# Performance work log

Measured on AMD Instinct MI355X. Metric: run time of the kernel, lower is better.

## Reference

```python
import jax, jax.numpy as jnp
import numpy as np

HEADS = 16
EPS = 1e-6

def _rmsnorm(x, g):
    # x: (..., d); norm = ||x||_2 * d^-0.5 (matches torch.norm-based RMSNorm)
    d = x.shape[-1]
    nrm = jnp.linalg.norm(x, axis=-1, keepdims=True) * (d ** -0.5)
    return x / (nrm + EPS) * g

def _rope(x, cos, sin):
    # x: (b,n,h,d) -> complex pairs over last dim; cos/sin: (1,n,1,d//2)
    b, n, h, d = x.shape
    xr = x.reshape(b, n, h, d // 2, 2)
    re, im = xr[..., 0], xr[..., 1]
    out_re = re * cos - im * sin
    out_im = re * sin + im * cos
    return jnp.stack([out_re, out_im], axis=-1).reshape(b, n, h, d)

def setup_inputs() -> dict:
    key = jax.random.key(0)
    ks = jax.random.split(key, 8)
    b, n, dim = 4, 4096, 1024
    d = dim // HEADS
    x = jax.random.normal(ks[0], (b, n, dim), dtype=jnp.float32)
    # rope freqs as cos/sin of random angles (broadcast shape 1,n,1,d//2)
    ang = jax.random.uniform(ks[1], (1, n, 1, d // 2), dtype=jnp.float32) * (2 * np.pi)
    freqs_cos = jnp.cos(ang)
    freqs_sin = jnp.sin(ang)
    sc = dim ** -0.5
    w_qkv = jax.random.normal(ks[2], (dim, 3 * dim), dtype=jnp.float32) * sc
    g_q = jnp.ones((d,), dtype=jnp.float32)
    g_k = jnp.ones((d,), dtype=jnp.float32)
    w_proj = jax.random.normal(ks[3], (dim, dim), dtype=jnp.float32) * sc
    b_proj = jnp.zeros((dim,), dtype=jnp.float32)
    return {"x": x, "freqs_cos": freqs_cos, "freqs_sin": freqs_sin,
            "w_qkv": w_qkv, "g_q": g_q, "g_k": g_k,
            "w_proj": w_proj, "b_proj": b_proj}

def reference(x, freqs_cos, freqs_sin, w_qkv, g_q, g_k, w_proj, b_proj):
    b, n, dim = x.shape
    h = HEADS
    d = dim // h
    scale = d ** -0.5
    qkv = x @ w_qkv  # (b,n,3*dim)
    q, k, v = jnp.split(qkv, 3, axis=-1)
    q = q.reshape(b, n, h, d)
    k = k.reshape(b, n, h, d)
    v = v.reshape(b, n, h, d)
    q = _rmsnorm(q, g_q)
    k = _rmsnorm(k, g_k)
    q = _rope(q, freqs_cos, freqs_sin)
    k = _rope(k, freqs_cos, freqs_sin)
    # per-token head-mixing attention: (b,n,h,h)
    attn = jnp.einsum('bnhd,bngd->bnhg', q, k) * scale
    attn = jax.nn.softmax(attn, axis=-1)
    out = jnp.einsum('bnhg,bngd->bnhd', attn, v).reshape(b, n, dim)
    return out @ w_proj + b_proj
```

## Files before the change

kernel.cpp:

```cpp
#include <hip/hip_runtime.h>
#include <hip/hip_bf16.h>
#include <stddef.h>

#define NTOK   16384
#define SEQN   4096
#define DIM    1024
#define K3     3072
#define HEADS  16
#define HD     64

typedef __attribute__((ext_vector_type(8)))  short  short8;
typedef __attribute__((ext_vector_type(4)))  float  float4v;

static __device__ __forceinline__ unsigned short f32_to_bf16_bits(float f) {
    unsigned u = __float_as_uint(f);
    unsigned r = u + 0x7fffu + ((u >> 16) & 1u);
    return (unsigned short)(r >> 16);
}
static __device__ __forceinline__ unsigned pack_bf16x2(float lo, float hi) {
    return (unsigned)f32_to_bf16_bits(lo) | ((unsigned)f32_to_bf16_bits(hi) << 16);
}
static __device__ __forceinline__ void unpack_bf16x8(uint4 u, float* f) {
    f[0] = __uint_as_float(u.x << 16); f[1] = __uint_as_float(u.x & 0xffff0000u);
    f[2] = __uint_as_float(u.y << 16); f[3] = __uint_as_float(u.y & 0xffff0000u);
    f[4] = __uint_as_float(u.z << 16); f[5] = __uint_as_float(u.z & 0xffff0000u);
    f[6] = __uint_as_float(u.w << 16); f[7] = __uint_as_float(u.w & 0xffff0000u);
}

typedef const void __attribute__((address_space(1)))* gas_ptr;
typedef void __attribute__((address_space(3)))* las_ptr;
static __device__ __forceinline__ void gload_lds16(const unsigned short* g,
                                                   unsigned short* l) {
    __builtin_amdgcn_global_load_lds((gas_ptr)g, (las_ptr)l, 16, 0, 0);
}

__global__ void cvt_f32_bf16(const float4* __restrict__ in,
                             ushort4* __restrict__ out, int n4) {
    int i = blockIdx.x * blockDim.x + threadIdx.x;
    if (i < n4) {
        float4 v = in[i];
        ushort4 o;
        o.x = f32_to_bf16_bits(v.x);
        o.y = f32_to_bf16_bits(v.y);
        o.z = f32_to_bf16_bits(v.z);
        o.w = f32_to_bf16_bits(v.w);
        out[i] = o;
    }
}

__global__ void transpose_cvt(const float* __restrict__ in,
                              unsigned short* __restrict__ out,
                              int K, int N) {
    __shared__ float t[32][33];
    int n0 = blockIdx.x * 32, k0 = blockIdx.y * 32;
    int tx = threadIdx.x, ty = threadIdx.y;
    #pragma unroll
    for (int r = ty; r < 32; r += 8)
        t[r][tx] = in[(size_t)(k0 + r) * N + n0 + tx];
    __syncthreads();
    #pragma unroll
    for (int r = ty; r < 32; r += 8)
        out[(size_t)(n0 + r) * K + k0 + tx] = f32_to_bf16_bits(t[tx][r]);
}

template<int WITH_BIAS>
__global__ __launch_bounds__(512, 2) void gemm_bf16_256(
    const unsigned short* __restrict__ A,
    const unsigned short* __restrict__ Bt,
    void* __restrict__ Cout,
    const float* __restrict__ bias,
    int M, int N)
{
    constexpr int K = 1024;
    __shared__ unsigned short As[2][256][64];
    __shared__ unsigned short Bs[2][256][64];

    const int tid  = threadIdx.x;
    const int wave = tid >> 6;
    const int lane = tid & 63;
    const int wm   = wave >> 2;
    const int wn   = wave & 3;
    const int l15  = lane & 15;
    const int l4   = lane >> 4;
    const int l7   = lane & 7;

    const int nwg = (int)gridDim.x;
    const int bid = (int)blockIdx.x;
    const int swz = (bid & 7) * (nwg >> 3) + (bid >> 3);
    const int ntn = N >> 8;
    const int rowBase = (swz / ntn) << 8;
    const int colBase = (swz % ntn) << 8;
    (void)M;

    const int drow = lane >> 3;
    const int lc   = l7 ^ drow;
    const unsigned short* gA = A  + (size_t)(rowBase + drow) * K + lc * 8;
    const unsigned short* gB = Bt + (size_t)(colBase + drow) * K + lc * 8;

    float4v acc[8][4];
    #pragma unroll
    for (int m = 0; m < 8; m++)
        #pragma unroll
        for (int n = 0; n < 4; n++) acc[m][n] = (float4v)0.0f;

    short8 aF[4][2], b0F[2][2], b1F[2][2];

#define STG_A(f, oddH, T) do {                                               \
    const int ra_ = ((wave >> 2) * 128) + (oddH) * 64 + (wave & 3) * 16;     \
    gload_lds16(gA + (size_t)(ra_    ) * K + (size_t)(T) * 64, &As[f][ra_    ][0]); \
    gload_lds16(gA + (size_t)(ra_ + 8) * K + (size_t)(T) * 64, &As[f][ra_ + 8][0]); \
  } while (0)
#define STG_B(f, oddH, T) do {                                               \
    const int rb_ = ((wave >> 1) * 64) + (oddH) * 32 + (wave & 1) * 16;      \
    gload_lds16(gB + (size_t)(rb_    ) * K + (size_t)(T) * 64, &Bs[f][rb_    ][0]); \
    gload_lds16(gB + (size_t)(rb_ + 8) * K + (size_t)(T) * 64, &Bs[f][rb_ + 8][0]); \
  } while (0)

#define RD_A(f, a) do {                                                      \
    _Pragma("unroll")                                                        \
    for (int ra = 0; ra < 4; ra++) {                                         \
      const unsigned short* r_ = &As[f][wm * 128 + (a) * 64 + ra * 16 + l15][0]; \
      aF[ra][0] = *(const short8*)(r_ + (((    l4) ^ l7) * 8));              \
      aF[ra][1] = *(const short8*)(r_ + (((4 + l4) ^ l7) * 8));              \
    } } while (0)
#define RD_B(f, b, dst) do {                                                 \
    _Pragma("unroll")                                                        \
    for (int cb = 0; cb < 2; cb++) {                                         \
      const unsigned short* r_ = &Bs[f][wn * 64 + (b) * 32 + cb * 16 + l15][0]; \
      dst[cb][0] = *(const short8*)(r_ + (((    l4) ^ l7) * 8));             \
      dst[cb][1] = *(const short8*)(r_ + (((4 + l4) ^ l7) * 8));             \
    } } while (0)

#define MM(a, b, bF) do {                                                    \
    _Pragma("unroll")                                                        \
    for (int ra = 0; ra < 4; ra++)                                           \
      _Pragma("unroll")                                                      \
      for (int cb = 0; cb < 2; cb++) {                                       \
        acc[(a)*4+ra][(b)*2+cb] = __builtin_amdgcn_mfma_f32_16x16x32_bf16(   \
            aF[ra][0], bF[cb][0], acc[(a)*4+ra][(b)*2+cb], 0, 0, 0);         \
        acc[(a)*4+ra][(b)*2+cb] = __builtin_amdgcn_mfma_f32_16x16x32_bf16(   \
            aF[ra][1], bF[cb][1], acc[(a)*4+ra][(b)*2+cb], 0, 0, 0);         \
      } } while (0)

#define BAR()   __builtin_amdgcn_s_barrier()
#define VM(n)   asm volatile("s_waitcnt vmcnt(" #n ")" ::: "memory")
#define P1()    __builtin_amdgcn_s_setprio(1)
#define P0()    __builtin_amdgcn_s_setprio(0)

    STG_A(0,0,0); STG_B(0,0,0); STG_B(0,1,0); STG_A(0,1,0);
    STG_A(1,0,1); STG_B(1,0,1); STG_B(1,1,1);
    VM(6);
    BAR();

    #pragma unroll 1
    for (int i = 0; i < 7; i++) {
        const int t1 = 2 * i + 1;
        RD_A(0,0); RD_B(0,0,b0F); STG_A(1,1,t1);
        BAR(); P1(); MM(0,0,b0F); P0(); BAR();
        RD_B(0,1,b1F);            STG_A(0,0,t1+1);
        BAR(); P1(); MM(0,1,b1F); P0(); BAR();
        RD_A(0,1);                STG_B(0,0,t1+1);
        BAR(); P1(); MM(1,1,b1F); P0(); BAR();
                                  STG_B(0,1,t1+1); VM(6);
        BAR(); P1(); MM(1,0,b0F); P0(); BAR();
        RD_A(1,0); RD_B(1,0,b0F); STG_A(0,1,t1+1);
        BAR(); P1(); MM(0,0,b0F); P0(); BAR();
        RD_B(1,1,b1F);            STG_A(1,0,t1+2);
        BAR(); P1(); MM(0,1,b1F); P0(); BAR();
        RD_A(1,1);                STG_B(1,0,t1+2);
        BAR(); P1(); MM(1,1,b1F); P0(); BAR();
                                  STG_B(1,1,t1+2); VM(6);
        BAR(); P1(); MM(1,0,b0F); P0(); BAR();
    }

    {
        RD_A(0,0); RD_B(0,0,b0F); STG_A(1,1,15);
        BAR(); P1(); MM(0,0,b0F); P0(); BAR();
        RD_B(0,1,b1F);
        BAR(); P1(); MM(0,1,b1F); P0(); BAR();
        RD_A(0,1);
        BAR(); P1(); MM(1,1,b1F); P0(); BAR();
        VM(0);
        BAR(); P1(); MM(1,0,b0F); P0(); BAR();
        RD_A(1,0); RD_B(1,0,b0F); P1(); MM(0,0,b0F); P0();
        RD_B(1,1,b1F);            P1(); MM(0,1,b1F); P0();
        RD_A(1,1);                P1(); MM(1,1,b1F); P0();
                                  P1(); MM(1,0,b0F); P0();
    }

    #pragma unroll
    for (int m = 0; m < 8; m++) {
        const int row = rowBase + wm * 128 + m * 16 + l4 * 4;
        #pragma unroll
        for (int n = 0; n < 4; n++) {
            const int col = colBase + wn * 64 + n * 16 + l15;
            if (WITH_BIAS) {
                const float bv = bias[col];
                #pragma unroll
                for (int r = 0; r < 4; r++)
                    ((float*)Cout)[(size_t)(row + r) * N + col] = acc[m][n][r] + bv;
            } else {
                #pragma unroll
                for (int r = 0; r < 4; r++)
                    ((unsigned short*)Cout)[(size_t)(row + r) * N + col] =
                        f32_to_bf16_bits(acc[m][n][r]);
            }
        }
    }
#undef STG_A
#undef STG_B
#undef RD_A
#undef RD_B
#undef MM
#undef BAR
#undef VM
#undef P1
#undef P0
}

__global__ __launch_bounds__(256) void attn_tok(
    const unsigned short* __restrict__ qkv,
    const float* __restrict__ fcos,
    const float* __restrict__ fsin,
    const float* __restrict__ gq,
    const float* __restrict__ gk,
    unsigned short* __restrict__ outb)
{
    __shared__ float kl[4][16][68];
    __shared__ float vl[4][16][68];

    const int tid  = threadIdx.x;
    const int wv   = tid >> 6;
    const int lane = tid & 63;
    const int h    = lane & 15;
    const int p    = lane >> 4;
    const int tok  = blockIdx.x * 4 + wv;
    const int n    = tok & (SEQN - 1);

    const unsigned short* base = qkv + (size_t)tok * K3 + h * 64 + p * 16;
    uint4 qr0 = *(const uint4*)(base);
    uint4 qr1 = *(const uint4*)(base + 8);
    uint4 kr0 = *(const uint4*)(base + DIM);
    uint4 kr1 = *(const uint4*)(base + DIM + 8);
    uint4 vr0 = *(const uint4*)(base + 2 * DIM);
    uint4 vr1 = *(const uint4*)(base + 2 * DIM + 8);

    float q[16], k[16], v[16];
    unpack_bf16x8(qr0, q); unpack_bf16x8(qr1, q + 8);
    unpack_bf16x8(kr0, k); unpack_bf16x8(kr1, k + 8);
    unpack_bf16x8(vr0, v); unpack_bf16x8(vr1, v + 8);

    float ssq = 0.f, ssk = 0.f;
    #pragma unroll
    for (int i = 0; i < 16; i++) { ssq += q[i] * q[i]; ssk += k[i] * k[i]; }
    ssq += __shfl_xor(ssq, 16); ssq += __shfl_xor(ssq, 32);
    ssk += __shfl_xor(ssk, 16); ssk += __shfl_xor(ssk, 32);
    const float sq = 1.0f / (sqrtf(ssq) * 0.125f + 1e-6f);
    const float sk = 1.0f / (sqrtf(ssk) * 0.125f + 1e-6f);

    #pragma unroll
    for (int c = 0; c < 4; c++) {
        float4 gg = *(const float4*)(gq + p * 16 + c * 4);
        float4 gh = *(const float4*)(gk + p * 16 + c * 4);
        q[c*4+0] *= sq * gg.x; q[c*4+1] *= sq * gg.y;
        q[c*4+2] *= sq * gg.z; q[c*4+3] *= sq * gg.w;
        k[c*4+0] *= sk * gh.x; k[c*4+1] *= sk * gh.y;
        k[c*4+2] *= sk * gh.z; k[c*4+3] *= sk * gh.w;
    }

    {
        const float* cb = fcos + n * 32 + p * 8;
        const float* sb = fsin + n * 32 + p * 8;
        float4 c0 = *(const float4*)cb, c1 = *(const float4*)(cb + 4);
        float4 s0 = *(const float4*)sb, s1 = *(const float4*)(sb + 4);
        float cs[8] = {c0.x,c0.y,c0.z,c0.w,c1.x,c1.y,c1.z,c1.w};
        float sn[8] = {s0.x,s0.y,s0.z,s0.w,s1.x,s1.y,s1.z,s1.w};
        #pragma unroll
        for (int j = 0; j < 8; j++) {
            float re = q[2*j], im = q[2*j+1];
            q[2*j]   = re * cs[j] - im * sn[j];
            q[2*j+1] = re * sn[j] + im * cs[j];
            re = k[2*j]; im = k[2*j+1];
            k[2*j]   = re * cs[j] - im * sn[j];
            k[2*j+1] = re * sn[j] + im * cs[j];
        }
    }

    {
        float* krow = &kl[wv][h][p * 16];
        float* vrow = &vl[wv][h][p * 16];
        #pragma unroll
        for (int c = 0; c < 4; c++) {
            *(float4*)(krow + c*4) = make_float4(k[c*4], k[c*4+1], k[c*4+2], k[c*4+3]);
            *(float4*)(vrow + c*4) = make_float4(v[c*4], v[c*4+1], v[c*4+2], v[c*4+3]);
        }
    }

    float s[16];
    #pragma unroll
    for (int g = 0; g < 16; g++) {
        const float* kg = &kl[wv][g][p * 16];
        float4 a0 = *(const float4*)(kg);
        float4 a1 = *(const float4*)(kg + 4);
        float4 a2 = *(const float4*)(kg + 8);
        float4 a3 = *(const float4*)(kg + 12);
        s[g] = q[0]*a0.x + q[1]*a0.y + q[2]*a0.z + q[3]*a0.w
             + q[4]*a1.x + q[5]*a1.y + q[6]*a1.z + q[7]*a1.w
             + q[8]*a2.x + q[9]*a2.y + q[10]*a2.z + q[11]*a2.w
             + q[12]*a3.x + q[13]*a3.y + q[14]*a3.z + q[15]*a3.w;
    }
    #pragma unroll
    for (int g = 0; g < 16; g++) {
        s[g] += __shfl_xor(s[g], 16);
        s[g] += __shfl_xor(s[g], 32);
        s[g] *= 0.125f;
    }

    float m = s[0];
    #pragma unroll
    for (int g = 1; g < 16; g++) m = fmaxf(m, s[g]);
    float sum = 0.f;
    #pragma unroll
    for (int g = 0; g < 16; g++) { s[g] = __expf(s[g] - m); sum += s[g]; }
    const float inv = 1.0f / sum;

    float o[16];
    #pragma unroll
    for (int i = 0; i < 16; i++) o[i] = 0.f;
    #pragma unroll
    for (int g = 0; g < 16; g++) {
        const float pg = s[g] * inv;
        const float* vg = &vl[wv][g][p * 16];
        float4 b0 = *(const float4*)(vg);
        float4 b1 = *(const float4*)(vg + 4);
        float4 b2 = *(const float4*)(vg + 8);
        float4 b3 = *(const float4*)(vg + 12);
        o[0]  += pg * b0.x; o[1]  += pg * b0.y; o[2]  += pg * b0.z; o[3]  += pg * b0.w;
        o[4]  += pg * b1.x; o[5]  += pg * b1.y; o[6]  += pg * b1.z; o[7]  += pg * b1.w;
        o[8]  += pg * b2.x; o[9]  += pg * b2.y; o[10] += pg * b2.z; o[11] += pg * b2.w;
        o[12] += pg * b3.x; o[13] += pg * b3.y; o[14] += pg * b3.z; o[15] += pg * b3.w;
    }

    uint4 r0, r1;
    r0.x = pack_bf16x2(o[0],  o[1]);  r0.y = pack_bf16x2(o[2],  o[3]);
    r0.z = pack_bf16x2(o[4],  o[5]);  r0.w = pack_bf16x2(o[6],  o[7]);
    r1.x = pack_bf16x2(o[8],  o[9]);  r1.y = pack_bf16x2(o[10], o[11]);
    r1.z = pack_bf16x2(o[12], o[13]); r1.w = pack_bf16x2(o[14], o[15]);
    unsigned short* ob = outb + (size_t)tok * DIM + h * 64 + p * 16;
    *(uint4*)(ob)     = r0;
    *(uint4*)(ob + 8) = r1;
}

extern "C" void kernel_launch(void* const* d_in, const int* in_sizes, int n_in,
                              void* d_out, int out_size, void* d_ws, size_t ws_size,
                              hipStream_t stream) {
    const float* x      = (const float*)d_in[0];
    const float* fcos   = (const float*)d_in[1];
    const float* fsin   = (const float*)d_in[2];
    const float* w_qkv  = (const float*)d_in[3];
    const float* g_q    = (const float*)d_in[4];
    const float* g_k    = (const float*)d_in[5];
    const float* w_proj = (const float*)d_in[6];
    const float* b_proj = (const float*)d_in[7];
    float* out = (float*)d_out;

    char* ws = (char*)d_ws;
    unsigned short* xb      = (unsigned short*)(ws);
    unsigned short* wqkvT   = (unsigned short*)(ws + 33554432);
    unsigned short* wprojT  = (unsigned short*)(ws + 39845888);
    unsigned short* qkv     = (unsigned short*)(ws + 41943040);
    unsigned short* attnout = (unsigned short*)(ws + 142606336);
    (void)ws_size; (void)in_sizes; (void)n_in; (void)out_size;

    {
        int n4 = (NTOK * DIM) / 4;
        cvt_f32_bf16<<<(n4 + 255) / 256, 256, 0, stream>>>(
            (const float4*)x, (ushort4*)xb, n4);
        transpose_cvt<<<dim3(K3 / 32, DIM / 32), dim3(32, 8), 0, stream>>>(
            w_qkv, wqkvT, DIM, K3);
        transpose_cvt<<<dim3(DIM / 32, DIM / 32), dim3(32, 8), 0, stream>>>(
            w_proj, wprojT, DIM, DIM);
    }
    gemm_bf16_256<0><<<dim3((NTOK / 256) * (K3 / 256)), 512, 0, stream>>>(
        xb, wqkvT, (void*)qkv, nullptr, NTOK, K3);
    attn_tok<<<NTOK / 4, 256, 0, stream>>>(qkv, fcos, fsin, g_q, g_k, attnout);
    gemm_bf16_256<1><<<dim3((NTOK / 256) * (DIM / 256)), 512, 0, stream>>>(
        attnout, wprojT, (void*)out, b_proj, NTOK, DIM);
}
```

Baseline: 332.8 us.

## Restructure GEMM main loop to overlap LDS reads with MFMA, halve barriers

Reworks the software pipeline of the bf16 MFMA GEMM main loop. Shared-memory fragment reads for the next sub-tile and global-to-LDS staging are now issued right after each MFMA cluster, with one barrier per phase instead of two. The prologue stages one extra tile and preloads the first fragments. Scheduling barriers keep the compiler from reordering across phases. This cuts barrier stalls and hides LDS latency behind MFMA work, but it risks LDS read/write hazards if the buffer-reuse ordering is wrong.

```diff
diff --git a/kernel.cpp b/kernel.cpp
--- a/kernel.cpp
+++ b/kernel.cpp
@@ -143,50 +143,46 @@
       } } while (0)
 
 #define BAR()   __builtin_amdgcn_s_barrier()
+#define SB()    __builtin_amdgcn_sched_barrier(0)
 #define VM(n)   asm volatile("s_waitcnt vmcnt(" #n ")" ::: "memory")
 #define P1()    __builtin_amdgcn_s_setprio(1)
 #define P0()    __builtin_amdgcn_s_setprio(0)
 
     STG_A(0,0,0); STG_B(0,0,0); STG_B(0,1,0); STG_A(0,1,0);
-    STG_A(1,0,1); STG_B(1,0,1); STG_B(1,1,1);
-    VM(6);
+    STG_A(1,0,1); STG_B(1,0,1); STG_B(1,1,1); STG_A(1,1,1);
+    VM(8);
     BAR();
+    RD_A(0,0); RD_B(0,0,b0F);
+    SB(); BAR();
 
     #pragma unroll 1
     for (int i = 0; i < 7; i++) {
-        const int t1 = 2 * i + 1;
-        RD_A(0,0); RD_B(0,0,b0F); STG_A(1,1,t1);
-        BAR(); P1(); MM(0,0,b0F); P0(); BAR();
-        RD_B(0,1,b1F);            STG_A(0,0,t1+1);
-        BAR(); P1(); MM(0,1,b1F); P0(); BAR();
-        RD_A(0,1);                STG_B(0,0,t1+1);
-        BAR(); P1(); MM(1,1,b1F); P0(); BAR();
-                                  STG_B(0,1,t1+1); VM(6);
-        BAR(); P1(); MM(1,0,b0F); P0(); BAR();
-        RD_A(1,0); RD_B(1,0,b0F); STG_A(0,1,t1+1);
-        BAR(); P1(); MM(0,0,b0F); P0(); BAR();
-        RD_B(1,1,b1F);            STG_A(1,0,t1+2);
-        BAR(); P1(); MM(0,1,b1F); P0(); BAR();
-        RD_A(1,1);                STG_B(1,0,t1+2);
-        BAR(); P1(); MM(1,1,b1F); P0(); BAR();
-                                  STG_B(1,1,t1+2); VM(6);
-        BAR(); P1(); MM(1,0,b0F); P0(); BAR();
-    }
-
-    {
-        RD_A(0,0); RD_B(0,0,b0F); STG_A(1,1,15);
-        BAR(); P1(); MM(0,0,b0F); P0(); BAR();
-        RD_B(0,1,b1F);
-        BAR(); P1(); MM(0,1,b1F); P0(); BAR();
-        RD_A(0,1);
-        BAR(); P1(); MM(1,1,b1F); P0(); BAR();
-        VM(0);
-        BAR(); P1(); MM(1,0,b0F); P0(); BAR();
-        RD_A(1,0); RD_B(1,0,b0F); P1(); MM(0,0,b0F); P0();
-        RD_B(1,1,b1F);            P1(); MM(0,1,b1F); P0();
-        RD_A(1,1);                P1(); MM(1,1,b1F); P0();
-                                  P1(); MM(1,0,b0F); P0();
-    }
+        const int T0 = 2 * i + 2, T1 = 2 * i + 3;
+        RD_B(0,1,b1F);                 STG_A(0,0,T0);
+        P1(); MM(0,0,b0F); P0(); SB(); BAR();
+        P1(); MM(0,1,b1F); P0(); RD_A(0,1);  STG_B(0,0,T0); SB(); BAR();
+        P1(); MM(1,1,b1F); P0();             STG_B(0,1,T0); SB(); BAR();
+        P1(); MM(1,0,b0F); P0(); VM(6);
+        RD_A(1,0); RD_B(1,0,b0F);            STG_A(0,1,T0); SB(); BAR();
+        RD_B(1,1,b1F);                 STG_A(1,0,T1);
+        P1(); MM(0,0,b0F); P0(); SB(); BAR();
+        P1(); MM(0,1,b1F); P0(); RD_A(1,1);  STG_B(1,0,T1); SB(); BAR();
+        P1(); MM(1,1,b1F); P0();             STG_B(1,1,T1); SB(); BAR();
+        P1(); MM(1,0,b0F); P0(); VM(6);
+        RD_A(0,0); RD_B(0,0,b0F);            STG_A(1,1,T1); SB(); BAR();
+    }
+
+    RD_B(0,1,b1F);
+    P1(); MM(0,0,b0F); P0(); SB(); BAR();
+    P1(); MM(0,1,b1F); P0(); RD_A(0,1); SB(); BAR();
+    P1(); MM(1,1,b1F); P0(); SB(); BAR();
+    P1(); MM(1,0,b0F); P0(); VM(0); SB(); BAR();
+    RD_A(1,0); RD_B(1,0,b0F);
+    RD_B(1,1,b1F);
+    P1(); MM(0,0,b0F); P0();
+    P1(); MM(0,1,b1F); P0(); RD_A(1,1);
+    P1(); MM(1,1,b1F); P0();
+    P1(); MM(1,0,b0F); P0();
 
     #pragma unroll
     for (int m = 0; m < 8; m++) {
@@ -213,6 +209,7 @@
 #undef RD_B
 #undef MM
 #undef BAR
+#undef SB
 #undef VM
 #undef P1
 #undef P0
```

Result: no change. 330.2 us (-0.8%).
